# Performance work log

Hardware: AMD Instinct MI355X
Metric: run time of the kernel (lower is better)

Reference implementation:

```python
import jax, jax.numpy as jnp
import numpy as np

IN_DIM = 512
MEM_DIM = 512
B = 4            # branching factor
LEAVES = 16384   # perfect B-ary tree => N = (B*LEAVES - 1) // (B - 1)


def _build_tree():
    # level sizes from leaves up to root; nodes laid out level-by-level
    sizes = []
    n = LEAVES
    while n >= 1:
        sizes.append(n)
        if n == 1:
            break
        n //= B
    N = sum(sizes)
    children = -np.ones((N, B), dtype=np.int32)
    off_prev, off = 0, sizes[0]
    for l in range(1, len(sizes)):
        nl = sizes[l]
        children[off:off + nl] = off_prev + np.arange(nl * B, dtype=np.int32).reshape(nl, B)
        off_prev, off = off, off + nl
    return N, children


def setup_inputs() -> dict:
    key = jax.random.key(0)
    ks = jax.random.split(key, 9)
    N, children = _build_tree()
    sx = 1.0 / np.sqrt(IN_DIM)
    sh = 1.0 / np.sqrt(MEM_DIM)
    return {
        "x": jax.random.normal(ks[0], (N, IN_DIM), dtype=jnp.float32),
        "children": jnp.asarray(children),
        "W_ioux": jax.random.normal(ks[1], (IN_DIM, 3 * MEM_DIM), dtype=jnp.float32) * sx,
        "b_ioux": jax.random.normal(ks[2], (3 * MEM_DIM,), dtype=jnp.float32) * sx,
        "W_iouh": jax.random.normal(ks[3], (MEM_DIM, 3 * MEM_DIM), dtype=jnp.float32) * sh,
        "b_iouh": jax.random.normal(ks[4], (3 * MEM_DIM,), dtype=jnp.float32) * sh,
        "W_fx": jax.random.normal(ks[5], (IN_DIM, MEM_DIM), dtype=jnp.float32) * sx,
        "b_fx": jax.random.normal(ks[6], (MEM_DIM,), dtype=jnp.float32) * sx,
        "W_fh": jax.random.normal(ks[7], (MEM_DIM, MEM_DIM), dtype=jnp.float32) * sh,
        "b_fh": jax.random.normal(ks[8], (MEM_DIM,), dtype=jnp.float32) * sh,
    }


def _level_sizes(N, Bf):
    sizes = []
    n = (N * (Bf - 1) + 1) // Bf  # leaf count of a perfect Bf-ary tree
    while n >= 1:
        sizes.append(n)
        if n == 1:
            break
        n //= Bf
    return sizes


def reference(x, children, W_ioux, b_ioux, W_iouh, b_iouh, W_fx, b_fx, W_fh, b_fh):
    N, Bf = children.shape
    M = W_iouh.shape[0]
    sizes = _level_sizes(N, Bf)  # static Python ints

    # precompute input-side linears for ALL nodes in two big GEMMs
    x_iou = x @ W_ioux + b_ioux          # [N, 3M]
    x_f = x @ W_fx + b_fx                # [N, M]

    h_all = jnp.zeros((N, M), dtype=x.dtype)
    c_all = jnp.zeros((N, M), dtype=x.dtype)

    off = 0
    for l, nl in enumerate(sizes):
        xi = x_iou[off:off + nl]                        # [nl, 3M]
        xf = x_f[off:off + nl]                          # [nl, M]
        if l == 0:
            # leaves: single zero child (matches torch zeros(1, mem_dim))
            ch_h = jnp.zeros((nl, 1, M), dtype=x.dtype)
            ch_c = jnp.zeros((nl, 1, M), dtype=x.dtype)
        else:
            idx = children[off:off + nl]                # [nl, B]
            ch_h = h_all[idx]                           # [nl, B, M]
            ch_c = c_all[idx]
        h_sum = ch_h.sum(axis=1)                        # [nl, M]
        iou = xi + h_sum @ W_iouh + b_iouh              # [nl, 3M]
        i, o, u = jnp.split(iou, 3, axis=1)
        i = jax.nn.sigmoid(i)
        o = jax.nn.sigmoid(o)
        u = jnp.tanh(u)
        # forget gate per child: sigmoid(fh(h_k) + fx(x))
        f = jax.nn.sigmoid(jnp.einsum('nkm,mp->nkp', ch_h, W_fh) + b_fh + xf[:, None, :])
        c = i * u + (f * ch_c).sum(axis=1)              # [nl, M]
        h = o * jnp.tanh(c)
        h_all = h_all.at[off:off + nl].set(h)
        c_all = c_all.at[off:off + nl].set(c)
        off += nl

    return h_all[N - 1:N]  # root hidden state, [1, M]
```

## Files before the change

kernel.cpp:

```cpp
#include <hip/hip_runtime.h>
#include <cstdint>

using short8 = __attribute__((ext_vector_type(8))) short;
using f32x4  = __attribute__((ext_vector_type(4))) float;
typedef unsigned short ushort_t;

__device__ __forceinline__ ushort_t f2bf(float f) {
    union { float f; unsigned int u; } v; v.f = f;
    unsigned int r = v.u + 0x7FFFu + ((v.u >> 16) & 1u);
    return (ushort_t)(r >> 16);
}
__device__ __forceinline__ float bf2f(ushort_t s) {
    union { unsigned int u; float f; } v; v.u = ((unsigned int)s) << 16;
    return v.f;
}
__device__ __forceinline__ float sigmoidf(float x) { return 1.f / (1.f + expf(-x)); }

__device__ __forceinline__ void async_copy16(void* lds, const void* g) {
    __builtin_amdgcn_global_load_lds((__attribute__((address_space(1))) void*)g,
                                     (__attribute__((address_space(3))) void*)lds,
                                     16, 0, 0);
}

#define KA 1024
#define KB 1536
#define NLEAF 16384
#define NNODE 21845
#define NINT  5461

#define OFF_WTIOUX  0UL
#define OFF_WTIOUH  (OFF_WTIOUX + 1536UL*KB*2)
#define OFF_WTFX    (OFF_WTIOUH + 1536UL*KB*2)
#define OFF_WTFH    (OFF_WTFX   + 512UL*KB*2)
#define OFF_BIASIOU (OFF_WTFH   + 512UL*KB*2)
#define OFF_BIASF   (OFF_BIASIOU + 1536UL*4)
#define OFF_XHL     (OFF_BIASF  + 512UL*4)
#define OFF_XF      (OFF_XHL    + 21848UL*KA*2)
#define OFF_HSUM    (OFF_XF     + 5464UL*512*4)
#define OFF_C32     (OFF_HSUM   + 4096UL*KA*2)
#define OFF_FC      (OFF_C32    + 16384UL*512*4)
#define OFF_IOU     (OFF_FC     + 4096UL*512*4)

__global__ void wsplit_kernel(const float* __restrict__ in, ushort_t* __restrict__ out, int N) {
    __shared__ float t[32][33];
    int kb = blockIdx.x * 32, nb = blockIdx.y * 32;
    for (int i = threadIdx.y; i < 32; i += 8)
        t[i][threadIdx.x] = in[(size_t)(kb + i) * N + nb + threadIdx.x];
    __syncthreads();
    for (int i = threadIdx.y; i < 32; i += 8) {
        float v = t[threadIdx.x][i];
        ushort_t hi = f2bf(v);
        ushort_t lo = f2bf(v - bf2f(hi));
        size_t row = (size_t)(nb + i) * KB + kb + threadIdx.x;
        out[row]        = hi;
        out[row + 512]  = hi;
        out[row + 1024] = lo;
    }
}

__global__ void bias_kernel(const float* __restrict__ b_ioux, const float* __restrict__ b_iouh,
                            const float* __restrict__ b_fx, const float* __restrict__ b_fh,
                            float* __restrict__ bias_iou, float* __restrict__ bias_f) {
    int t = blockIdx.x * blockDim.x + threadIdx.x;
    if (t < 1536) bias_iou[t] = b_ioux[t] + b_iouh[t];
    if (t < 512)  bias_f[t]   = b_fx[t] + b_fh[t];
}

__global__ void xexp_kernel(const float* __restrict__ x, ushort_t* __restrict__ xe, int n4) {
    int t = blockIdx.x * blockDim.x + threadIdx.x;
    if (t >= n4) return;
    int j = t >> 7, m4 = (t & 127) * 4;
    float4 v = *(const float4*)&x[(size_t)j * 512 + m4];
    ushort4 hi, lo;
    hi.x = f2bf(v.x); lo.x = f2bf(v.x - bf2f(hi.x));
    hi.y = f2bf(v.y); lo.y = f2bf(v.y - bf2f(hi.y));
    hi.z = f2bf(v.z); lo.z = f2bf(v.z - bf2f(hi.z));
    hi.w = f2bf(v.w); lo.w = f2bf(v.w - bf2f(hi.w));
    ushort_t* row = xe + (size_t)j * KA;
    *(ushort4*)&row[m4] = hi;
    *(ushort4*)&row[512 + m4] = lo;
}

__global__ void hsum_kernel(const ushort_t* __restrict__ h_hl, ushort_t* __restrict__ hsum_hl,
                            int n4) {
    int t = blockIdx.x * blockDim.x + threadIdx.x;
    if (t >= n4) return;
    int j = t >> 7, m4 = (t & 127) * 4;
    const ushort_t* base = h_hl + (size_t)(4 * j) * KA;
    float s0 = 0.f, s1 = 0.f, s2 = 0.f, s3 = 0.f;
#pragma unroll
    for (int r = 0; r < 4; ++r) {
        ushort4 h4 = *(const ushort4*)&base[(size_t)r * KA + m4];
        ushort4 l4 = *(const ushort4*)&base[(size_t)r * KA + 512 + m4];
        s0 += bf2f(h4.x) + bf2f(l4.x);
        s1 += bf2f(h4.y) + bf2f(l4.y);
        s2 += bf2f(h4.z) + bf2f(l4.z);
        s3 += bf2f(h4.w) + bf2f(l4.w);
    }
    ushort4 hi, lo;
    hi.x = f2bf(s0); lo.x = f2bf(s0 - bf2f(hi.x));
    hi.y = f2bf(s1); lo.y = f2bf(s1 - bf2f(hi.y));
    hi.z = f2bf(s2); lo.z = f2bf(s2 - bf2f(hi.z));
    hi.w = f2bf(s3); lo.w = f2bf(s3 - bf2f(hi.w));
    ushort_t* row = hsum_hl + (size_t)j * KA;
    *(ushort4*)&row[m4] = hi;
    *(ushort4*)&row[512 + m4] = lo;
}

template <int MODE>
__global__ __launch_bounds__(256)
void gemm_kernel(int M,
                 const ushort_t* __restrict__ a1,
                 const ushort_t* __restrict__ a2,
                 const ushort_t* __restrict__ b1, const ushort_t* __restrict__ b2,
                 float* __restrict__ outf, ushort_t* __restrict__ outb, int ldout,
                 const float* __restrict__ c_prev, const float* __restrict__ xf,
                 const float* __restrict__ bias_f) {
    __shared__ __align__(16) ushort_t Al[128 * 32];
    __shared__ __align__(16) ushort_t Bl[128 * 32];

    const int tid  = threadIdx.x;
    const int lane = tid & 63, wv = tid >> 6;
    const int l15  = lane & 15, quad = lane >> 4;
    const int wm   = wv >> 1, wn = wv & 1;
    const int m0   = blockIdx.x * 128;
    const int n0   = blockIdx.y * 128;

    const int srow = wv * 16 + (lane >> 2);
    const int kch  = ((lane & 3) ^ ((lane >> 3) & 3)) * 8;
    const int swz  = (quad ^ ((l15 >> 1) & 3)) * 8;

    const ushort_t* a1p[2]; const ushort_t* a2p[2];
    const ushort_t* b1p[2]; const ushort_t* b2p[2];
#pragma unroll
    for (int r = 0; r < 2; ++r) {
        int rl = m0 + srow + r * 64; if (rl > M - 1) rl = M - 1;
        a1p[r] = a1 + (size_t)rl * KA + kch;
        a2p[r] = a2 ? a2 + (size_t)rl * KA + kch : nullptr;
        int nb = n0 + srow + r * 64;
        b1p[r] = b1 + (size_t)nb * KB + kch;
        b2p[r] = b2 ? b2 + (size_t)nb * KB + kch : nullptr;
    }

    f32x4 acc[4][4] = {};
    const int nphase = a2 ? 2 : 1;
    for (int ph = 0; ph < nphase; ++ph) {
        for (int k0 = 0; k0 < KB; k0 += 32) {
            int ka = (k0 < KA) ? k0 : k0 - KA;
            __syncthreads();
#pragma unroll
            for (int r = 0; r < 2; ++r) {
                async_copy16(&Al[(size_t)(wv * 16 + r * 64) * 32], (ph ? a2p[r] : a1p[r]) + ka);
                async_copy16(&Bl[(size_t)(wv * 16 + r * 64) * 32], (ph ? b2p[r] : b1p[r]) + k0);
            }
            __syncthreads();

            short8 aF[4], bF[4];
#pragma unroll
            for (int i = 0; i < 4; ++i) {
                aF[i] = *(const short8*)&Al[(size_t)(wm * 64 + i * 16 + l15) * 32 + swz];
                bF[i] = *(const short8*)&Bl[(size_t)(wn * 64 + i * 16 + l15) * 32 + swz];
            }
#pragma unroll
            for (int i = 0; i < 4; ++i)
#pragma unroll
                for (int j = 0; j < 4; ++j)
                    acc[i][j] = __builtin_amdgcn_mfma_f32_16x16x32_bf16(aF[i], bF[j], acc[i][j], 0, 0, 0);
        }
    }

    if constexpr (MODE == 0 || MODE == 2) {
#pragma unroll
        for (int i = 0; i < 4; ++i) {
            int mbase = m0 + wm * 64 + i * 16 + quad * 4;
#pragma unroll
            for (int j = 0; j < 4; ++j) {
                int n = n0 + wn * 64 + j * 16 + l15;
#pragma unroll
                for (int r = 0; r < 4; ++r) {
                    int m = mbase + r;
                    if (m < M) {
                        if constexpr (MODE == 0) outf[(size_t)m * ldout + n] = acc[i][j][r];
                        else                     outb[(size_t)m * ldout + n] = f2bf(acc[i][j][r]);
                    }
                }
            }
        }
    } else {
#pragma unroll
        for (int i = 0; i < 4; ++i) {
            int mbase = m0 + wm * 64 + i * 16 + quad * 4;
            if (mbase < M) {
                int jg = mbase >> 2;
#pragma unroll
                for (int j = 0; j < 4; ++j) {
                    int n = n0 + wn * 64 + j * 16 + l15;
                    float add = xf[(size_t)jg * 512 + n] + bias_f[n];
                    float fc = 0.f;
#pragma unroll
                    for (int r = 0; r < 4; ++r) {
                        float f = sigmoidf(acc[i][j][r] + add);
                        fc += f * c_prev[(size_t)(mbase + r) * 512 + n];
                    }
                    outf[(size_t)jg * 512 + n] = fc;
                }
            }
        }
    }
}

template <bool IOU_BF>
__global__ void cell_kernel(const void* __restrict__ iou_v, const float* __restrict__ bias_iou,
                            const float* __restrict__ fc,
                            ushort_t* __restrict__ h_hl, float* __restrict__ c32,
                            int row_off, int n4, float* __restrict__ out) {
    int t = blockIdx.x * blockDim.x + threadIdx.x;
    if (t >= n4) return;
    int j = t >> 7, m4 = (t & 127) * 4;
    float pi[4], po[4], pu[4];
    if constexpr (IOU_BF) {
        const ushort_t* row = (const ushort_t*)iou_v + (size_t)j * 1536;
        ushort4 a = *(const ushort4*)&row[m4];
        ushort4 b = *(const ushort4*)&row[512 + m4];
        ushort4 c = *(const ushort4*)&row[1024 + m4];
        pi[0]=bf2f(a.x); pi[1]=bf2f(a.y); pi[2]=bf2f(a.z); pi[3]=bf2f(a.w);
        po[0]=bf2f(b.x); po[1]=bf2f(b.y); po[2]=bf2f(b.z); po[3]=bf2f(b.w);
        pu[0]=bf2f(c.x); pu[1]=bf2f(c.y); pu[2]=bf2f(c.z); pu[3]=bf2f(c.w);
    } else {
        const float* row = (const float*)iou_v + (size_t)j * 1536;
        float4 a = *(const float4*)&row[m4];
        float4 b = *(const float4*)&row[512 + m4];
        float4 c = *(const float4*)&row[1024 + m4];
        pi[0]=a.x; pi[1]=a.y; pi[2]=a.z; pi[3]=a.w;
        po[0]=b.x; po[1]=b.y; po[2]=b.z; po[3]=b.w;
        pu[0]=c.x; pu[1]=c.y; pu[2]=c.z; pu[3]=c.w;
    }
    float4 bi = *(const float4*)&bias_iou[m4];
    float4 bo = *(const float4*)&bias_iou[512 + m4];
    float4 bu = *(const float4*)&bias_iou[1024 + m4];
    float4 fcv = fc ? *(const float4*)&fc[(size_t)j * 512 + m4]
                    : float4{0.f, 0.f, 0.f, 0.f};
    float bia[4] = {bi.x, bi.y, bi.z, bi.w};
    float boa[4] = {bo.x, bo.y, bo.z, bo.w};
    float bua[4] = {bu.x, bu.y, bu.z, bu.w};
    float fca[4] = {fcv.x, fcv.y, fcv.z, fcv.w};
    float cv[4], hv[4];
#pragma unroll
    for (int q = 0; q < 4; ++q) {
        float iv = sigmoidf(pi[q] + bia[q]);
        float ov = sigmoidf(po[q] + boa[q]);
        float uv = tanhf(  pu[q] + bua[q]);
        cv[q] = iv * uv + fca[q];
        hv[q] = ov * tanhf(cv[q]);
    }
    size_t g = (size_t)(row_off + j);
    *(float4*)&c32[g * 512 + m4] = float4{cv[0], cv[1], cv[2], cv[3]};
    ushort4 hi, lo;
    hi.x = f2bf(hv[0]); lo.x = f2bf(hv[0] - bf2f(hi.x));
    hi.y = f2bf(hv[1]); lo.y = f2bf(hv[1] - bf2f(hi.y));
    hi.z = f2bf(hv[2]); lo.z = f2bf(hv[2] - bf2f(hi.z));
    hi.w = f2bf(hv[3]); lo.w = f2bf(hv[3] - bf2f(hi.w));
    ushort_t* hr = h_hl + g * KA;
    *(ushort4*)&hr[m4] = hi;
    *(ushort4*)&hr[512 + m4] = lo;
    if (out) *(float4*)&out[m4] = float4{hv[0], hv[1], hv[2], hv[3]};
}

extern "C" void kernel_launch(void* const* d_in, const int* in_sizes, int n_in,
                              void* d_out, int out_size, void* d_ws, size_t ws_size,
                              hipStream_t stream) {
    const float* x       = (const float*)d_in[0];
    const float* W_ioux  = (const float*)d_in[2];
    const float* b_ioux  = (const float*)d_in[3];
    const float* W_iouh  = (const float*)d_in[4];
    const float* b_iouh  = (const float*)d_in[5];
    const float* W_fx    = (const float*)d_in[6];
    const float* b_fx    = (const float*)d_in[7];
    const float* W_fh    = (const float*)d_in[8];
    const float* b_fh    = (const float*)d_in[9];
    float* out = (float*)d_out;
    char* ws = (char*)d_ws;

    ushort_t* WTioux = (ushort_t*)(ws + OFF_WTIOUX);
    ushort_t* WTiouh = (ushort_t*)(ws + OFF_WTIOUH);
    ushort_t* WTfx   = (ushort_t*)(ws + OFF_WTFX);
    ushort_t* WTfh   = (ushort_t*)(ws + OFF_WTFH);
    float*    bias_iou = (float*)(ws + OFF_BIASIOU);
    float*    bias_f   = (float*)(ws + OFF_BIASF);
    ushort_t* x_hl   = (ushort_t*)(ws + OFF_XHL);
    ushort_t* h_hl   = x_hl;
    float*    xf32   = (float*)(ws + OFF_XF);
    ushort_t* hsum_hl= (ushort_t*)(ws + OFF_HSUM);
    float*    c32    = (float*)(ws + OFF_C32);
    float*    fc_buf = (float*)(ws + OFF_FC);
    float*    iou32  = (float*)(ws + OFF_IOU);
    ushort_t* iou_bf = (ushort_t*)(ws + OFF_IOU);

    wsplit_kernel<<<dim3(16, 48), dim3(32, 8), 0, stream>>>(W_ioux, WTioux, 1536);
    wsplit_kernel<<<dim3(16, 48), dim3(32, 8), 0, stream>>>(W_iouh, WTiouh, 1536);
    wsplit_kernel<<<dim3(16, 16), dim3(32, 8), 0, stream>>>(W_fx,   WTfx,   512);
    wsplit_kernel<<<dim3(16, 16), dim3(32, 8), 0, stream>>>(W_fh,   WTfh,   512);
    bias_kernel<<<6, 256, 0, stream>>>(b_ioux, b_iouh, b_fx, b_fh, bias_iou, bias_f);

    xexp_kernel<<<(NNODE * 128 + 255) / 256, 256, 0, stream>>>(x, x_hl, NNODE * 128);

    gemm_kernel<0><<<dim3(43, 4), 256, 0, stream>>>(
        NINT, x_hl + (size_t)NLEAF * KA, nullptr, WTfx, nullptr,
        xf32, nullptr, 512, nullptr, nullptr, nullptr);

    for (int q = 0; q < 2; ++q) {
        int node_off = q * 8192;
        gemm_kernel<2><<<dim3(64, 12), 256, 0, stream>>>(
            8192, x_hl + (size_t)node_off * KA, nullptr, WTioux, nullptr,
            nullptr, iou_bf, 1536, nullptr, nullptr, nullptr);
        cell_kernel<true><<<(8192 * 128) / 256, 256, 0, stream>>>(
            iou_bf, bias_iou, nullptr, h_hl, c32, node_off, 8192 * 128, nullptr);
    }

    const int sizes[8] = {16384, 4096, 1024, 256, 64, 16, 4, 1};
    int off = 0;
    for (int l = 1; l < 8; ++l) {
        off += sizes[l - 1];
        int ioff = off - NLEAF;
        int nl = sizes[l];
        int M4 = 4 * nl;
        int n4 = nl * 128;

        hsum_kernel<<<(n4 + 255) / 256, 256, 0, stream>>>(h_hl, hsum_hl, n4);

        gemm_kernel<1><<<dim3((M4 + 127) / 128, 4), 256, 0, stream>>>(
            M4, h_hl, nullptr, WTfh, nullptr,
            fc_buf, nullptr, 512, c32, xf32 + (size_t)ioff * 512, bias_f);

        gemm_kernel<0><<<dim3((nl + 127) / 128, 12), 256, 0, stream>>>(
            nl, x_hl + (size_t)off * KA, hsum_hl, WTioux, WTiouh,
            iou32, nullptr, 1536, nullptr, nullptr, nullptr);

        cell_kernel<false><<<(n4 + 255) / 256, 256, 0, stream>>>(
            iou32, bias_iou, fc_buf, h_hl, c32, 0, n4, (l == 7) ? out : nullptr);
    }
    (void)d_in; (void)in_sizes; (void)n_in; (void)out_size; (void)ws_size;
}
```

Measured before the change: 881.1 us.

## Fuse IOU GEMM with LSTM cell epilogue and restructure h/c buffers

Replaces the separate IOU GEMM plus cell_kernel pair with one fused kernel. Each block computes matching i, o and u column tiles (three 64-wide slices) for 128 rows, then applies the gates, c and h in the epilogue. This removes the IOU intermediate write and read-back, including the bf16 leaf IOU buffer, and cuts several launches per level. Per-level h/c buffers are laid out separately and placed over already-consumed regions of the workspace. The trade-offs are a larger accumulator footprint per thread, with a risk to occupancy, and scattered scalar epilogue stores.

```diff
diff --git a/kernel.cpp b/kernel.cpp
--- a/kernel.cpp
+++ b/kernel.cpp
@@ -35,11 +35,11 @@
 #define OFF_BIASIOU (OFF_WTFH   + 512UL*KB*2)
 #define OFF_BIASF   (OFF_BIASIOU + 1536UL*4)
 #define OFF_XHL     (OFF_BIASF  + 512UL*4)
-#define OFF_XF      (OFF_XHL    + 21848UL*KA*2)
+#define OFF_HLEAF   (OFF_XHL    + 21848UL*KA*2)
+#define OFF_XF      (OFF_HLEAF  + 16384UL*KA*2)
 #define OFF_HSUM    (OFF_XF     + 5464UL*512*4)
-#define OFF_C32     (OFF_HSUM   + 4096UL*KA*2)
-#define OFF_FC      (OFF_C32    + 16384UL*512*4)
-#define OFF_IOU     (OFF_FC     + 4096UL*512*4)
+#define OFF_CLEAF   (OFF_HSUM   + 4096UL*KA*2)
+#define OFF_FC      (OFF_CLEAF  + 16384UL*512*4)
 
 __global__ void wsplit_kernel(const float* __restrict__ in, ushort_t* __restrict__ out, int N) {
     __shared__ float t[32][33];
@@ -113,7 +113,7 @@
                  const ushort_t* __restrict__ a1,
                  const ushort_t* __restrict__ a2,
                  const ushort_t* __restrict__ b1, const ushort_t* __restrict__ b2,
-                 float* __restrict__ outf, ushort_t* __restrict__ outb, int ldout,
+                 float* __restrict__ outf, int ldout,
                  const float* __restrict__ c_prev, const float* __restrict__ xf,
                  const float* __restrict__ bias_f) {
     __shared__ __align__(16) ushort_t Al[128 * 32];
@@ -169,7 +169,7 @@
         }
     }
 
-    if constexpr (MODE == 0 || MODE == 2) {
+    if constexpr (MODE == 0) {
 #pragma unroll
         for (int i = 0; i < 4; ++i) {
             int mbase = m0 + wm * 64 + i * 16 + quad * 4;
@@ -179,10 +179,7 @@
 #pragma unroll
                 for (int r = 0; r < 4; ++r) {
                     int m = mbase + r;
-                    if (m < M) {
-                        if constexpr (MODE == 0) outf[(size_t)m * ldout + n] = acc[i][j][r];
-                        else                     outb[(size_t)m * ldout + n] = f2bf(acc[i][j][r]);
-                    }
+                    if (m < M) outf[(size_t)m * ldout + n] = acc[i][j][r];
                 }
             }
         }
@@ -209,61 +206,101 @@
     }
 }
 
-template <bool IOU_BF>
-__global__ void cell_kernel(const void* __restrict__ iou_v, const float* __restrict__ bias_iou,
-                            const float* __restrict__ fc,
-                            ushort_t* __restrict__ h_hl, float* __restrict__ c32,
-                            int row_off, int n4, float* __restrict__ out) {
-    int t = blockIdx.x * blockDim.x + threadIdx.x;
-    if (t >= n4) return;
-    int j = t >> 7, m4 = (t & 127) * 4;
-    float pi[4], po[4], pu[4];
-    if constexpr (IOU_BF) {
-        const ushort_t* row = (const ushort_t*)iou_v + (size_t)j * 1536;
-        ushort4 a = *(const ushort4*)&row[m4];
-        ushort4 b = *(const ushort4*)&row[512 + m4];
-        ushort4 c = *(const ushort4*)&row[1024 + m4];
-        pi[0]=bf2f(a.x); pi[1]=bf2f(a.y); pi[2]=bf2f(a.z); pi[3]=bf2f(a.w);
-        po[0]=bf2f(b.x); po[1]=bf2f(b.y); po[2]=bf2f(b.z); po[3]=bf2f(b.w);
-        pu[0]=bf2f(c.x); pu[1]=bf2f(c.y); pu[2]=bf2f(c.z); pu[3]=bf2f(c.w);
-    } else {
-        const float* row = (const float*)iou_v + (size_t)j * 1536;
-        float4 a = *(const float4*)&row[m4];
-        float4 b = *(const float4*)&row[512 + m4];
-        float4 c = *(const float4*)&row[1024 + m4];
-        pi[0]=a.x; pi[1]=a.y; pi[2]=a.z; pi[3]=a.w;
-        po[0]=b.x; po[1]=b.y; po[2]=b.z; po[3]=b.w;
-        pu[0]=c.x; pu[1]=c.y; pu[2]=c.z; pu[3]=c.w;
-    }
-    float4 bi = *(const float4*)&bias_iou[m4];
-    float4 bo = *(const float4*)&bias_iou[512 + m4];
-    float4 bu = *(const float4*)&bias_iou[1024 + m4];
-    float4 fcv = fc ? *(const float4*)&fc[(size_t)j * 512 + m4]
-                    : float4{0.f, 0.f, 0.f, 0.f};
-    float bia[4] = {bi.x, bi.y, bi.z, bi.w};
-    float boa[4] = {bo.x, bo.y, bo.z, bo.w};
-    float bua[4] = {bu.x, bu.y, bu.z, bu.w};
-    float fca[4] = {fcv.x, fcv.y, fcv.z, fcv.w};
-    float cv[4], hv[4];
-#pragma unroll
-    for (int q = 0; q < 4; ++q) {
-        float iv = sigmoidf(pi[q] + bia[q]);
-        float ov = sigmoidf(po[q] + boa[q]);
-        float uv = tanhf(  pu[q] + bua[q]);
-        cv[q] = iv * uv + fca[q];
-        hv[q] = ov * tanhf(cv[q]);
-    }
-    size_t g = (size_t)(row_off + j);
-    *(float4*)&c32[g * 512 + m4] = float4{cv[0], cv[1], cv[2], cv[3]};
-    ushort4 hi, lo;
-    hi.x = f2bf(hv[0]); lo.x = f2bf(hv[0] - bf2f(hi.x));
-    hi.y = f2bf(hv[1]); lo.y = f2bf(hv[1] - bf2f(hi.y));
-    hi.z = f2bf(hv[2]); lo.z = f2bf(hv[2] - bf2f(hi.z));
-    hi.w = f2bf(hv[3]); lo.w = f2bf(hv[3] - bf2f(hi.w));
-    ushort_t* hr = h_hl + g * KA;
-    *(ushort4*)&hr[m4] = hi;
-    *(ushort4*)&hr[512 + m4] = lo;
-    if (out) *(float4*)&out[m4] = float4{hv[0], hv[1], hv[2], hv[3]};
+template <int NPH>
+__global__ __launch_bounds__(256)
+void fused_kernel(int M,
+                  const ushort_t* __restrict__ a1,
+                  const ushort_t* __restrict__ a2,
+                  const ushort_t* __restrict__ b1, const ushort_t* __restrict__ b2,
+                  const float* __restrict__ bias_iou,
+                  const float* __restrict__ fc,
+                  float* __restrict__ c_out,
+                  ushort_t* __restrict__ h_out,
+                  float* __restrict__ outp) {
+    __shared__ __align__(16) ushort_t Al[128 * 32];
+    __shared__ __align__(16) ushort_t Bl[3 * 64 * 32];
+
+    const int tid  = threadIdx.x;
+    const int lane = tid & 63, wv = tid >> 6;
+    const int l15  = lane & 15, quad = lane >> 4;
+    const int m0   = blockIdx.x * 128;
+    const int n0   = blockIdx.y * 64;
+
+    const int srow = wv * 16 + (lane >> 2);
+    const int kch  = ((lane & 3) ^ ((lane >> 3) & 3)) * 8;
+    const int swz  = (quad ^ ((l15 >> 1) & 3)) * 8;
+
+    const ushort_t* a1p[2]; const ushort_t* a2p[2];
+    const ushort_t* b1p[3]; const ushort_t* b2p[3];
+#pragma unroll
+    for (int r = 0; r < 2; ++r) {
+        int rl = m0 + srow + r * 64; if (rl > M - 1) rl = M - 1;
+        a1p[r] = a1 + (size_t)rl * KA + kch;
+        a2p[r] = (NPH == 2) ? a2 + (size_t)rl * KA + kch : nullptr;
+    }
+#pragma unroll
+    for (int g = 0; g < 3; ++g) {
+        int wrow = g * 512 + n0 + srow;
+        b1p[g] = b1 + (size_t)wrow * KB + kch;
+        b2p[g] = (NPH == 2) ? b2 + (size_t)wrow * KB + kch : nullptr;
+    }
+
+    f32x4 acc[3][2][4] = {};
+    for (int ph = 0; ph < NPH; ++ph) {
+        for (int k0 = 0; k0 < KB; k0 += 32) {
+            int ka = (k0 < KA) ? k0 : k0 - KA;
+            __syncthreads();
+#pragma unroll
+            for (int r = 0; r < 2; ++r)
+                async_copy16(&Al[(size_t)(wv * 16 + r * 64) * 32], (ph ? a2p[r] : a1p[r]) + ka);
+#pragma unroll
+            for (int g = 0; g < 3; ++g)
+                async_copy16(&Bl[(size_t)(g * 64 + wv * 16) * 32], (ph ? b2p[g] : b1p[g]) + k0);
+            __syncthreads();
+
+            short8 aF[2];
+#pragma unroll
+            for (int i = 0; i < 2; ++i)
+                aF[i] = *(const short8*)&Al[(size_t)(wv * 32 + i * 16 + l15) * 32 + swz];
+#pragma unroll
+            for (int g = 0; g < 3; ++g) {
+                short8 bF[4];
+#pragma unroll
+                for (int j = 0; j < 4; ++j)
+                    bF[j] = *(const short8*)&Bl[(size_t)(g * 64 + j * 16 + l15) * 32 + swz];
+#pragma unroll
+                for (int i = 0; i < 2; ++i)
+#pragma unroll
+                    for (int j = 0; j < 4; ++j)
+                        acc[g][i][j] = __builtin_amdgcn_mfma_f32_16x16x32_bf16(aF[i], bF[j], acc[g][i][j], 0, 0, 0);
+            }
+        }
+    }
+
+#pragma unroll
+    for (int i = 0; i < 2; ++i) {
+        int mbase = m0 + wv * 32 + i * 16 + quad * 4;
+#pragma unroll
+        for (int r = 0; r < 4; ++r) {
+            int m = mbase + r;
+            if (m < M) {
+#pragma unroll
+                for (int j = 0; j < 4; ++j) {
+                    int n = n0 + j * 16 + l15;
+                    float iv = sigmoidf(acc[0][i][j][r] + bias_iou[n]);
+                    float ov = sigmoidf(acc[1][i][j][r] + bias_iou[512 + n]);
+                    float uv = tanhf(  acc[2][i][j][r] + bias_iou[1024 + n]);
+                    float c = iv * uv + ((NPH == 2) ? fc[(size_t)m * 512 + n] : 0.f);
+                    float h = ov * tanhf(c);
+                    c_out[(size_t)m * 512 + n] = c;
+                    ushort_t hi = f2bf(h), lo = f2bf(h - bf2f(hi));
+                    h_out[(size_t)m * KA + n] = hi;
+                    h_out[(size_t)m * KA + 512 + n] = lo;
+                    if (outp && m == 0) outp[n] = h;
+                }
+            }
+        }
+    }
 }
 
 extern "C" void kernel_launch(void* const* d_in, const int* in_sizes, int n_in,
@@ -288,13 +325,13 @@
     float*    bias_iou = (float*)(ws + OFF_BIASIOU);
     float*    bias_f   = (float*)(ws + OFF_BIASF);
     ushort_t* x_hl   = (ushort_t*)(ws + OFF_XHL);
-    ushort_t* h_hl   = x_hl;
+    ushort_t* h_int  = x_hl;
+    ushort_t* h_leaf = (ushort_t*)(ws + OFF_HLEAF);
+    float*    c_int  = (float*)(ws + OFF_HLEAF);
     float*    xf32   = (float*)(ws + OFF_XF);
     ushort_t* hsum_hl= (ushort_t*)(ws + OFF_HSUM);
-    float*    c32    = (float*)(ws + OFF_C32);
+    float*    c_leaf = (float*)(ws + OFF_CLEAF);
     float*    fc_buf = (float*)(ws + OFF_FC);
-    float*    iou32  = (float*)(ws + OFF_IOU);
-    ushort_t* iou_bf = (ushort_t*)(ws + OFF_IOU);
 
     wsplit_kernel<<<dim3(16, 48), dim3(32, 8), 0, stream>>>(W_ioux, WTioux, 1536);
     wsplit_kernel<<<dim3(16, 48), dim3(32, 8), 0, stream>>>(W_iouh, WTiouh, 1536);
@@ -306,38 +343,37 @@
 
     gemm_kernel<0><<<dim3(43, 4), 256, 0, stream>>>(
         NINT, x_hl + (size_t)NLEAF * KA, nullptr, WTfx, nullptr,
-        xf32, nullptr, 512, nullptr, nullptr, nullptr);
-
-    for (int q = 0; q < 2; ++q) {
-        int node_off = q * 8192;
-        gemm_kernel<2><<<dim3(64, 12), 256, 0, stream>>>(
-            8192, x_hl + (size_t)node_off * KA, nullptr, WTioux, nullptr,
-            nullptr, iou_bf, 1536, nullptr, nullptr, nullptr);
-        cell_kernel<true><<<(8192 * 128) / 256, 256, 0, stream>>>(
-            iou_bf, bias_iou, nullptr, h_hl, c32, node_off, 8192 * 128, nullptr);
-    }
+        xf32, 512, nullptr, nullptr, nullptr);
+
+    fused_kernel<1><<<dim3(128, 8), 256, 0, stream>>>(
+        NLEAF, x_hl, nullptr, WTioux, nullptr, bias_iou,
+        nullptr, c_leaf, h_leaf, nullptr);
 
     const int sizes[8] = {16384, 4096, 1024, 256, 64, 16, 4, 1};
     int off = 0;
     for (int l = 1; l < 8; ++l) {
+        int off_prev = off;
         off += sizes[l - 1];
         int ioff = off - NLEAF;
         int nl = sizes[l];
         int M4 = 4 * nl;
         int n4 = nl * 128;
 
-        hsum_kernel<<<(n4 + 255) / 256, 256, 0, stream>>>(h_hl, hsum_hl, n4);
+        const ushort_t* child_h = (l == 1) ? h_leaf
+                                           : h_int + (size_t)(off_prev - NLEAF) * KA;
+        const float*    child_c = (l == 1) ? c_leaf
+                                           : c_int + (size_t)(off_prev - NLEAF) * 512;
+
+        hsum_kernel<<<(n4 + 255) / 256, 256, 0, stream>>>(child_h, hsum_hl, n4);
 
         gemm_kernel<1><<<dim3((M4 + 127) / 128, 4), 256, 0, stream>>>(
-            M4, h_hl, nullptr, WTfh, nullptr,
-            fc_buf, nullptr, 512, c32, xf32 + (size_t)ioff * 512, bias_f);
-
-        gemm_kernel<0><<<dim3((nl + 127) / 128, 12), 256, 0, stream>>>(
-            nl, x_hl + (size_t)off * KA, hsum_hl, WTioux, WTiouh,
-            iou32, nullptr, 1536, nullptr, nullptr, nullptr);
-
-        cell_kernel<false><<<(n4 + 255) / 256, 256, 0, stream>>>(
-            iou32, bias_iou, fc_buf, h_hl, c32, 0, n4, (l == 7) ? out : nullptr);
+            M4, child_h, nullptr, WTfh, nullptr,
+            fc_buf, 512, child_c, xf32 + (size_t)ioff * 512, bias_f);
+
+        fused_kernel<2><<<dim3((nl + 127) / 128, 8), 256, 0, stream>>>(
+            nl, x_hl + (size_t)off * KA, hsum_hl, WTioux, WTiouh, bias_iou,
+            fc_buf, c_int + (size_t)ioff * 512, h_int + (size_t)ioff * KA,
+            (l == 7) ? out : nullptr);
     }
     (void)d_in; (void)in_sizes; (void)n_in; (void)out_size; (void)ws_size;
 }
```

Result: slower. 1.075 ms (+22.0%).
